# Kernel tuning notes

Hardware: AMD Instinct MI355X
Metric: run time of the kernel (lower is better)

The kernel has to match this reference:

```python
import jax, jax.numpy as jnp
from jax import lax
import numpy as np

DIM = 768      # model dim
NL = 12        # num mamba layers
DS = 16        # d_state
DI = 1536      # d_inner = 2*dim
DC = 4         # d_conv
P = 16         # patch size
IMG = 256
NP = (IMG // P) ** 2  # 256 patches
GS = 5         # KAN grid_size
SO = 3         # KAN spline_order
NK = NL // 3   # 4 KAN layers
BATCH = 32


def setup_inputs() -> dict:
    key = jax.random.key(0)
    ks = jax.random.split(key, 16)
    def n(k, shape, s=0.02):
        return jax.random.normal(k, shape, jnp.float32) * s
    return {
        "x": jax.random.normal(ks[0], (BATCH, 3, IMG, IMG), jnp.float32),
        "patch_w": n(ks[1], (DIM, 3, P, P)),
        "patch_b": jnp.zeros((DIM,), jnp.float32),
        "pos_embed": n(ks[2], (1, NP, DIM)),
        "in_proj_w": n(ks[3], (NL, 2 * DI, DIM)),
        "conv_w": n(ks[4], (NL, DI, 1, DC), 0.1),
        "conv_b": jnp.zeros((NL, DI), jnp.float32),
        "x_proj_w": n(ks[5], (NL, 2 * DS, DI)),
        "dt_proj_w": n(ks[6], (NL, DS, DI)),
        "dt_proj_b": jnp.zeros((NL, DS), jnp.float32),
        "A_log": jnp.tile(jnp.log(jnp.arange(1, DS + 1, dtype=jnp.float32)), (NL, 1)),
        "D_param": jnp.ones((NL, DI), jnp.float32),
        "out_proj_w": n(ks[7], (NL, DIM, DI)),
        "kan_base_w": n(ks[8], (NK, DIM, DIM)),
        "kan_coeff": n(ks[9], (NK, DIM, DIM, GS + SO), 0.1),
        "kan_bias": n(ks[10], (NK, DIM), 0.01),
        "norm_w": jnp.ones((DIM,), jnp.float32),
        "norm_b": jnp.zeros((DIM,), jnp.float32),
    }


def _mamba_block(x, in_w, cw, cb, xpw, dtw, dtb, alog, Dp, ow):
    Bsz, L, _ = x.shape
    xr = jnp.einsum('bld,ed->ble', x, in_w)              # [B,L,2*DI]
    x1, res = xr[..., :DI], xr[..., DI:]
    # causal depthwise conv (pad d_conv-1 on left, truncate to L)
    xc = lax.conv_general_dilated(
        x1.transpose(0, 2, 1), cw, (1,), [(DC - 1, 0)],
        feature_group_count=DI,
        dimension_numbers=('NCH', 'OIH', 'NCH')) + cb[None, :, None]
    x1 = jax.nn.silu(xc.transpose(0, 2, 1))              # [B,L,DI]
    x_dbl = jnp.einsum('bld,ed->ble', x1, xpw)           # [B,L,2*DS]
    Bp = x_dbl[..., DS:]                                 # dt half of x_proj is discarded (as in torch)
    dt = jax.nn.softplus(jnp.einsum('bld,nd->bln', x1, dtw) + dtb)  # [B,L,DS]
    A = -jnp.exp(alog)                                   # [DS]
    Ad = jnp.exp(A * dt)                                 # [B,L,DS]
    u = x1[..., :DI // DS].mean(-1)                      # [B,L]
    Bd = dt * Bp * u[..., None]                          # [B,L,DS]
    def step(s, ab):
        a, b = ab
        s = s * a + b
        return s, s
    _, ys = lax.scan(step, jnp.zeros((Bsz, DS), x.dtype),
                     (Ad.transpose(1, 0, 2), Bd.transpose(1, 0, 2)))
    y = ys.transpose(1, 0, 2)                            # [B,L,DS]
    y = jnp.repeat(y, DI // DS, axis=-1)                 # n -> (n d)
    y = y + x1 * Dp
    y = y * jax.nn.silu(res)
    return jnp.einsum('bld,ed->ble', y, ow)              # [B,L,DIM]


def _kan(xf, bw, coeff, bias):
    base = xf @ bw.T + bias
    grid = jnp.linspace(-1.0, 1.0, GS + 1)
    denom = grid[1:] - grid[:-1] + 1e-8
    xs = (xf[..., None] - grid[:-1]) / denom             # [M,DIM,GS]
    basis = jnp.where((xs >= 0) & (xs < 1), xs, 0.0)
    return base + jnp.einsum('bik,oik->bo', basis, coeff[:, :, :GS])


def reference(x, patch_w, patch_b, pos_embed, in_proj_w, conv_w, conv_b,
              x_proj_w, dt_proj_w, dt_proj_b, A_log, D_param, out_proj_w,
              kan_base_w, kan_coeff, kan_bias, norm_w, norm_b):
    Bsz = x.shape[0]
    h = lax.conv_general_dilated(
        x, patch_w, (P, P), 'VALID',
        dimension_numbers=('NCHW', 'OIHW', 'NCHW')) + patch_b[None, :, None, None]
    h = h.transpose(0, 2, 3, 1).reshape(Bsz, NP, DIM) + pos_embed
    for i in range(NL):
        h = _mamba_block(h, in_proj_w[i], conv_w[i], conv_b[i], x_proj_w[i],
                         dt_proj_w[i], dt_proj_b[i], A_log[i], D_param[i], out_proj_w[i])
        if i % 3 == 2 and i // 3 < NK:
            j = i // 3
            hf = h.reshape(-1, DIM)
            h = _kan(hf, kan_base_w[j], kan_coeff[j], kan_bias[j]).reshape(Bsz, NP, DIM) + h
    mu = h.mean(-1, keepdims=True)
    var = ((h - mu) ** 2).mean(-1, keepdims=True)
    return (h - mu) / jnp.sqrt(var + 1e-5) * norm_w + norm_b
```

## Files before the change

### kernel.cpp

```cpp
#include <hip/hip_runtime.h>

#define BATCH 32
#define NPATCH 256
#define MROWS (BATCH * NPATCH)
#define DIM 768
#define DI 1536
#define DS 16

typedef __bf16 bf16_t;
typedef __attribute__((ext_vector_type(8))) __bf16 bf16x8;
typedef __attribute__((ext_vector_type(4))) float floatx4;

__device__ __forceinline__ float bf2f(unsigned short u) {
    union { unsigned int i; float f; } v; v.i = ((unsigned int)u) << 16; return v.f;
}
__device__ __forceinline__ unsigned short f2bf(float f) {
    union { float f; unsigned int i; } u; u.f = f;
    unsigned int r = u.i + 0x7FFFu + ((u.i >> 16) & 1u);
    return (unsigned short)(r >> 16);
}
__device__ __forceinline__ float ldin(const void* p, int i, int bf) {
    if (bf) return bf2f(((const unsigned short*)p)[i]);
    return ((const float*)p)[i];
}
__device__ __forceinline__ float4 ldin4(const void* p, int i, int bf) {
    if (bf) {
        ushort4 u = *(const ushort4*)((const unsigned short*)p + i);
        return make_float4(bf2f(u.x), bf2f(u.y), bf2f(u.z), bf2f(u.w));
    }
    return *(const float4*)((const float*)p + i);
}
__device__ __forceinline__ float siluf(float x) { return x / (1.0f + expf(-x)); }

__global__ void detect_k(const void* alog, int* flag) {
    if (threadIdx.x == 0 && blockIdx.x == 0) {
        float v = ((const float*)alog)[1];
        flag[0] = (fabsf(v - 0.69314718f) < 0.01f) ? 0 : 1;
    }
}

__global__ __launch_bounds__(256) void cvt4_k(const int* __restrict__ flag,
                                              const void* __restrict__ in,
                                              unsigned short* __restrict__ out, int n4) {
    int i = blockIdx.x * 256 + threadIdx.x;
    if (i >= n4) return;
    float4 v = ldin4(in, i * 4, flag[0]);
    ushort4 o;
    o.x = f2bf(v.x); o.y = f2bf(v.y); o.z = f2bf(v.z); o.w = f2bf(v.w);
    *(ushort4*)(out + i * 4) = o;
}

__global__ __launch_bounds__(256) void kcoef_k(const int* __restrict__ flag,
                                               const void* __restrict__ co,
                                               bf16_t* __restrict__ out) {
    int idx = blockIdx.x * 256 + threadIdx.x;
    int bf = flag[0];
    int j = idx / (768 * 3840);
    int r = idx - j * (768 * 3840);
    int n = r / 3840;
    int kk = r - n * 3840;
    int i = kk / 5, k5 = kk - i * 5;
    out[idx] = (bf16_t)ldin(co, ((j * 768 + n) * 768 + i) * 8 + k5, bf);
}

__global__ __launch_bounds__(256) void wproj_k(const int* __restrict__ flag,
                                               const void* __restrict__ dtw,
                                               const void* __restrict__ xpw,
                                               bf16_t* __restrict__ w2) {
    int idx = blockIdx.x * 256 + threadIdx.x;
    int bf = flag[0];
    int i = idx / (128 * 1536);
    int r = idx - i * (128 * 1536);
    int n = r / 1536, k = r - n * 1536;
    float v;
    if (n < 16)       v = ldin(dtw, (i * 16 + n) * 1536 + k, bf);
    else if (n < 32)  v = ldin(xpw, (i * 32 + n) * 1536 + k, bf);
    else if (n == 32) v = (k < 96) ? (1.0f / 96.0f) : 0.0f;
    else              v = 0.0f;
    w2[idx] = (bf16_t)v;
}

__global__ __launch_bounds__(256) void cvtconv_k(const int* __restrict__ flag,
                                                 const void* __restrict__ cw,
                                                 bf16_t* __restrict__ cwr) {
    int idx = blockIdx.x * 256 + threadIdx.x;
    int bf = flag[0];
    int i = idx / (4 * 1536);
    int r = idx - i * (4 * 1536);
    int k = r / 1536, c = r - k * 1536;
    cwr[idx] = (bf16_t)ldin(cw, i * 1536 * 4 + c * 4 + k, bf);
}

__global__ __launch_bounds__(256) void basis_k(const bf16_t* __restrict__ h,
                                               bf16_t* __restrict__ bas) {
    int idx = blockIdx.x * 256 + threadIdx.x;
    int m = idx / 96, i8 = (idx - m * 96) * 8;
    bf16x8 hv = *(const bf16x8*)(h + (size_t)m * 768 + i8);
    union { bf16_t a[40]; bf16x8 v[5]; } ob;
#pragma unroll
    for (int ii = 0; ii < 8; ii++) {
        float xv = (float)hv[ii];
#pragma unroll
        for (int k5 = 0; k5 < 5; k5++) {
            float tt = (xv + 1.0f - 0.4f * (float)k5) * 2.5f;
            ob.a[ii * 5 + k5] = (bf16_t)((tt >= 0.0f && tt < 1.0f) ? tt : 0.0f);
        }
    }
    bf16_t* op = bas + (size_t)m * 3840 + (size_t)i8 * 5;
#pragma unroll
    for (int j = 0; j < 5; j++) *(bf16x8*)(op + j * 8) = ob.v[j];
}

__global__ __launch_bounds__(256) void im2col_k(const int* __restrict__ flag,
                                                const void* __restrict__ x,
                                                bf16_t* __restrict__ xp) {
    int idx = blockIdx.x * 256 + threadIdx.x;
    int bf = flag[0];
    int m = idx / 768, kc = idx - m * 768;
    int b = m >> 8, p = m & 255;
    int py = p >> 4, px = p & 15;
    int c = kc >> 8, rr = kc & 255;
    int ky = rr >> 4, kx = rr & 15;
    int src = ((b * 3 + c) * 256 + py * 16 + ky) * 256 + px * 16 + kx;
    xp[idx] = (bf16_t)ldin(x, src, bf);
}

template<int DBUF>
__global__ __launch_bounds__(256) void mgemm_t(
    const bf16_t* __restrict__ A, int lda,
    const bf16_t* __restrict__ W, int ldw,
    bf16_t* __restrict__ C, int ldc,
    int K, int mode, int gx,
    const int* __restrict__ flag,
    const void* __restrict__ bias, int boff,
    const void* __restrict__ aux, int aoff,
    const bf16_t* __restrict__ H, int ldh,
    float* __restrict__ dtu) {
    __shared__ bf16_t sm[DBUF ? 2 : 1][2 * 128 * 64];
    const int t = threadIdx.x;
    const int lane = t & 63, wave = t >> 6;
    const int wm = wave >> 1, wn = wave & 1;

    int m0, n0, kbeg, kend;
    if (mode == 5) {
        int mt = blockIdx.x >> 2, ks = blockIdx.x & 3;
        m0 = mt << 7; n0 = 0;
        int KS = K >> 2;
        kbeg = ks * KS; kend = kbeg + KS;
    } else {
        const int bid = blockIdx.x;
        const int xcd = bid & 7, l = bid >> 3;
        const int w = gx < 8 ? gx : 8;
        const int cb8 = w * 8;
        const int ch = l / cb8, rem = l - ch * cb8;
        const int mi = rem / w, ni = rem - mi * w;
        m0 = (xcd * 8 + mi) << 7;
        n0 = (ch * w + ni) << 7;
        kbeg = 0; kend = K;
    }

    const int srow = t >> 3;
    const int colperm = (((t & 7) ^ (srow & 7)) << 3);
    const bf16_t* gA[4]; const bf16_t* gB[4];
#pragma unroll
    for (int r = 0; r < 4; r++) {
        gA[r] = A + (size_t)(m0 + r * 32 + srow) * lda + colperm;
        gB[r] = W + (size_t)(n0 + r * 32 + srow) * ldw + colperm;
    }

    floatx4 acc[4][4];
#pragma unroll
    for (int i = 0; i < 4; i++)
#pragma unroll
        for (int j = 0; j < 4; j++) acc[i][j] = (floatx4){0.f, 0.f, 0.f, 0.f};

    const int kq = lane >> 4;
    const int mr = lane & 15;

    auto stage = [&](int buf, int kt) {
        char* sa = (char*)&sm[buf][0];
#pragma unroll
        for (int r = 0; r < 4; r++) {
            const int off = r * 4096 + wave * 1024;
            __builtin_amdgcn_global_load_lds(
                (const __attribute__((address_space(1))) unsigned int*)(gA[r] + kt),
                (__attribute__((address_space(3))) unsigned int*)(sa + off), 16, 0, 0);
            __builtin_amdgcn_global_load_lds(
                (const __attribute__((address_space(1))) unsigned int*)(gB[r] + kt),
                (__attribute__((address_space(3))) unsigned int*)(sa + 16384 + off), 16, 0, 0);
        }
    };

    auto compute = [&](int buf) {
        const bf16_t* sAc = &sm[buf][0];
        const bf16_t* sBc = sAc + 128 * 64;
#pragma unroll
        for (int half = 0; half < 2; half++) {
            const int cb = half * 4 + kq;
            if (mode == 5) {
                if (wn == 0) {
                    bf16x8 af[4], bw3[3];
#pragma unroll
                    for (int i = 0; i < 4; i++) {
                        int rw = wm * 64 + i * 16 + mr;
                        af[i] = *(const bf16x8*)(sAc + rw * 64 + ((cb ^ (rw & 7)) << 3));
                    }
#pragma unroll
                    for (int j = 0; j < 3; j++) {
                        int rw = j * 16 + mr;
                        bw3[j] = *(const bf16x8*)(sBc + rw * 64 + ((cb ^ (rw & 7)) << 3));
                    }
#pragma unroll
                    for (int i = 0; i < 4; i++)
#pragma unroll
                        for (int j = 0; j < 3; j++)
                            acc[i][j] = __builtin_amdgcn_mfma_f32_16x16x32_bf16(af[i], bw3[j], acc[i][j], 0, 0, 0);
                }
            } else {
                bf16x8 af[4], bw[4];
#pragma unroll
                for (int i = 0; i < 4; i++) {
                    int rw = wm * 64 + i * 16 + mr;
                    af[i] = *(const bf16x8*)(sAc + rw * 64 + ((cb ^ (rw & 7)) << 3));
                }
#pragma unroll
                for (int j = 0; j < 4; j++) {
                    int rw = wn * 64 + j * 16 + mr;
                    bw[j] = *(const bf16x8*)(sBc + rw * 64 + ((cb ^ (rw & 7)) << 3));
                }
#pragma unroll
                for (int i = 0; i < 4; i++)
#pragma unroll
                    for (int j = 0; j < 4; j++)
                        acc[i][j] = __builtin_amdgcn_mfma_f32_16x16x32_bf16(af[i], bw[j], acc[i][j], 0, 0, 0);
            }
        }
    };

    if (DBUF) {
        stage(0, kbeg);
        __syncthreads();
        int cur = 0;
        for (int kt = kbeg; kt < kend; kt += 64) {
            if (kt + 64 < kend) stage(cur ^ 1, kt + 64);
            compute(cur);
            __syncthreads();
            cur ^= 1;
        }
    } else {
        for (int kt = kbeg; kt < kend; kt += 64) {
            stage(0, kt);
            __syncthreads();
            compute(0);
            __syncthreads();
        }
    }

    const int col = lane & 15;
    const int rq = (lane >> 4) * 4;

    if (mode == 5) {
        if (wn == 0) {
            int ks = blockIdx.x & 3;
            float* dst = dtu + (size_t)ks * (MROWS * 64);
#pragma unroll
            for (int i = 0; i < 4; i++) {
#pragma unroll
                for (int reg = 0; reg < 4; reg++) {
                    int gm = m0 + wm * 64 + i * 16 + rq + reg;
#pragma unroll
                    for (int j = 0; j < 3; j++) {
                        int gn = j * 16 + col;
                        if (gn <= 32)
                            dst[(size_t)gm * 64 + gn] = acc[i][j][reg];
                    }
                }
            }
        }
        return;
    }

    const int bff = (mode == 1 || mode == 2) ? flag[0] : 0;
#pragma unroll
    for (int i = 0; i < 4; i++) {
#pragma unroll
        for (int reg = 0; reg < 4; reg++) {
            int gm = m0 + wm * 64 + i * 16 + rq + reg;
#pragma unroll
            for (int j = 0; j < 4; j++) {
                int gn = n0 + wn * 64 + j * 16 + col;
                float v = acc[i][j][reg];
                if (mode == 1) v += ldin(bias, boff + gn, bff) + ldin(aux, aoff + (gm & 255) * 768 + gn, bff);
                else if (mode == 2) v += ldin(bias, boff + gn, bff);
                else if (mode == 3) v += (float)C[(size_t)gm * ldc + gn] + (float)H[(size_t)gm * ldh + gn];
                C[(size_t)gm * ldc + gn] = (bf16_t)v;
            }
        }
    }
}

__global__ __launch_bounds__(256) void conv_k(const int* __restrict__ flag,
                                              const bf16_t* __restrict__ xr,
                                              const bf16_t* __restrict__ cwr,
                                              const void* __restrict__ cb, int cbo,
                                              bf16_t* __restrict__ xc) {
    int idx = blockIdx.x * 256 + threadIdx.x;
    int bf = flag[0];
    int m = idx / 192, c8 = (idx - m * 192) * 8;
    int l = m & 255;
    float acc[8];
    float4 b0 = ldin4(cb, cbo + c8, bf), b1 = ldin4(cb, cbo + c8 + 4, bf);
    acc[0] = b0.x; acc[1] = b0.y; acc[2] = b0.z; acc[3] = b0.w;
    acc[4] = b1.x; acc[5] = b1.y; acc[6] = b1.z; acc[7] = b1.w;
#pragma unroll
    for (int k = 0; k < 4; k++) {
        if (l + k - 3 >= 0) {
            bf16x8 xv = *(const bf16x8*)(xr + (size_t)(m + k - 3) * 3072 + c8);
            bf16x8 wv = *(const bf16x8*)(cwr + k * 1536 + c8);
#pragma unroll
            for (int j = 0; j < 8; j++) acc[j] += (float)xv[j] * (float)wv[j];
        }
    }
    bf16x8 o;
#pragma unroll
    for (int j = 0; j < 8; j++) o[j] = (bf16_t)siluf(acc[j]);
    *(bf16x8*)(xc + (size_t)m * 1536 + c8) = o;
}

__global__ __launch_bounds__(256) void scan_k(const int* __restrict__ flag,
                                              const float* __restrict__ dtu,
                                              const void* __restrict__ dtb, int dtbo,
                                              const void* __restrict__ alog, int alo,
                                              float* __restrict__ ys) {
    int wid = (blockIdx.x * 256 + threadIdx.x) >> 6;
    int lane = threadIdx.x & 63;
    int b = wid >> 4, s = wid & 15;
    int bf = flag[0];
    float dtbv = ldin(dtb, dtbo + s, bf);
    float Av = -expf(ldin(alog, alo + s, bf));
    const float* pb = dtu + (size_t)b * (256 * 64);
    float* yo = ys + (size_t)b * (256 * 16);
    float Aj[4], Bj[4];
    float A = 1.0f, Bv = 0.0f;
#pragma unroll
    for (int j = 0; j < 4; j++) {
        int l = lane * 4 + j;
        float rdt = dtbv, rBp = 0.0f, ru = 0.0f;
#pragma unroll
        for (int ks = 0; ks < 4; ks++) {
            const float* q = pb + (size_t)ks * (MROWS * 64) + (size_t)l * 64;
            rdt += q[s];
            rBp += q[16 + s];
            ru  += q[32];
        }
        float dt = (rdt > 20.0f) ? rdt : log1pf(expf(rdt));
        float a = expf(Av * dt);
        float bb = dt * rBp * ru;
        Bv = Bv * a + bb;
        A = A * a;
        Aj[j] = A; Bj[j] = Bv;
    }
#pragma unroll
    for (int off = 1; off < 64; off <<= 1) {
        float pa = __shfl_up(A, off);
        float pb2 = __shfl_up(Bv, off);
        if (lane >= off) { Bv = pb2 * A + Bv; A = pa * A; }
    }
    float ex = __shfl_up(Bv, 1);
    if (lane == 0) ex = 0.0f;
#pragma unroll
    for (int j = 0; j < 4; j++) {
        int l = lane * 4 + j;
        yo[l * 16 + s] = Aj[j] * ex + Bj[j];
    }
}

__global__ __launch_bounds__(256) void gate_k(const int* __restrict__ flag,
                                              const float* __restrict__ ys,
                                              bf16_t* __restrict__ xc,
                                              const bf16_t* __restrict__ xr,
                                              const void* __restrict__ Dp, int dpo) {
    int idx = blockIdx.x * 256 + threadIdx.x;
    int bf = flag[0];
    int m = idx / 192, d8 = (idx - m * 192) * 8;
    float yv = ys[m * 16 + d8 / 96];
    bf16x8 rv = *(const bf16x8*)(xr + (size_t)m * 3072 + 1536 + d8);
    bf16x8 xv = *(const bf16x8*)(xc + (size_t)m * 1536 + d8);
    float4 dp0 = ldin4(Dp, dpo + d8, bf), dp1 = ldin4(Dp, dpo + d8 + 4, bf);
    float dpv[8] = {dp0.x, dp0.y, dp0.z, dp0.w, dp1.x, dp1.y, dp1.z, dp1.w};
    bf16x8 o;
#pragma unroll
    for (int j = 0; j < 8; j++) {
        float v = yv + (float)xv[j] * dpv[j];
        o[j] = (bf16_t)(v * siluf((float)rv[j]));
    }
    *(bf16x8*)(xc + (size_t)m * 1536 + d8) = o;
}

__global__ __launch_bounds__(256) void lnorm_k(const int* __restrict__ flag,
                                               const bf16_t* __restrict__ h,
                                               const void* __restrict__ nw,
                                               const void* __restrict__ nb,
                                               void* __restrict__ out) {
    __shared__ float ls[4];
    int bf = flag[0];
    int m = blockIdx.x, t = threadIdx.x;
    const bf16_t* row = h + (size_t)m * 768;
    float v0 = (float)row[t], v1 = (float)row[t + 256], v2 = (float)row[t + 512];
    float s = v0 + v1 + v2;
#pragma unroll
    for (int o = 32; o; o >>= 1) s += __shfl_xor(s, o);
    if ((t & 63) == 0) ls[t >> 6] = s;
    __syncthreads();
    float mu = (ls[0] + ls[1] + ls[2] + ls[3]) * (1.0f / 768.0f);
    __syncthreads();
    float d0 = v0 - mu, d1 = v1 - mu, d2 = v2 - mu;
    float q = d0 * d0 + d1 * d1 + d2 * d2;
#pragma unroll
    for (int o = 32; o; o >>= 1) q += __shfl_xor(q, o);
    if ((t & 63) == 0) ls[t >> 6] = q;
    __syncthreads();
    float var = (ls[0] + ls[1] + ls[2] + ls[3]) * (1.0f / 768.0f);
    float inv = rsqrtf(var + 1e-5f);
    float vv[3] = {d0, d1, d2};
#pragma unroll
    for (int j = 0; j < 3; j++) {
        int colx = t + 256 * j;
        float o = vv[j] * inv * ldin(nw, colx, bf) + ldin(nb, colx, bf);
        size_t oi = (size_t)m * 768 + colx;
        if (bf) ((unsigned short*)out)[oi] = f2bf(o);
        else    ((float*)out)[oi] = o;
    }
}

extern "C" void kernel_launch(void* const* d_in, const int* in_sizes, int n_in,
                              void* d_out, int out_size, void* d_ws, size_t ws_size,
                              hipStream_t stream) {
    const void* x        = d_in[0];
    const void* patch_w  = d_in[1];
    const void* patch_b  = d_in[2];
    const void* pos      = d_in[3];
    const void* in_w     = d_in[4];
    const void* conv_w   = d_in[5];
    const void* conv_b   = d_in[6];
    const void* xpw      = d_in[7];
    const void* dtw      = d_in[8];
    const void* dtb      = d_in[9];
    const void* alog     = d_in[10];
    const void* Dp       = d_in[11];
    const void* out_w    = d_in[12];
    const void* kbw      = d_in[13];
    const void* kcoef    = d_in[14];
    const void* kbias    = d_in[15];
    const void* nw       = d_in[16];
    const void* nb       = d_in[17];

    char* base = (char*)d_ws;
    size_t off = 0;
    int* flag = (int*)base;                          off += 256;
    float* dtu  = (float*)(base + off);              off += (size_t)4 * MROWS * 64 * 4;
    float* ysb  = (float*)(base + off);              off += (size_t)MROWS * 16 * 4;
    bf16_t* hA  = (bf16_t*)(base + off);             off += (size_t)MROWS * DIM * 2;
    bf16_t* hB  = (bf16_t*)(base + off);             off += (size_t)MROWS * DIM * 2;
    bf16_t* xr  = (bf16_t*)(base + off);             off += (size_t)MROWS * 2 * DI * 2;
    bf16_t* xc  = (bf16_t*)(base + off);             off += (size_t)MROWS * DI * 2;
    bf16_t* wpatch = (bf16_t*)(base + off);          off += (size_t)DIM * DIM * 2;
    bf16_t* win  = (bf16_t*)(base + off);            off += (size_t)12 * 2 * DI * DIM * 2;
    bf16_t* wout = (bf16_t*)(base + off);            off += (size_t)12 * DIM * DI * 2;
    bf16_t* wkbw = (bf16_t*)(base + off);            off += (size_t)4 * DIM * DIM * 2;
    bf16_t* wkco = (bf16_t*)(base + off);            off += (size_t)4 * DIM * 3840 * 2;
    bf16_t* w2   = (bf16_t*)(base + off);            off += (size_t)12 * 128 * DI * 2;
    bf16_t* cwr  = (bf16_t*)(base + off);            off += (size_t)12 * 4 * DI * 2;
    bf16_t* basis = xr;
    bf16_t* im2c  = xr;

    detect_k<<<1, 64, 0, stream>>>(alog, flag);

    cvt4_k<<<(DIM * DIM / 4 + 255) / 256, 256, 0, stream>>>(flag, patch_w, (unsigned short*)wpatch, DIM * DIM / 4);
    cvt4_k<<<(12 * 2 * DI * DIM / 4 + 255) / 256, 256, 0, stream>>>(flag, in_w, (unsigned short*)win, 12 * 2 * DI * DIM / 4);
    cvt4_k<<<(12 * DIM * DI / 4 + 255) / 256, 256, 0, stream>>>(flag, out_w, (unsigned short*)wout, 12 * DIM * DI / 4);
    cvt4_k<<<(4 * DIM * DIM / 4 + 255) / 256, 256, 0, stream>>>(flag, kbw, (unsigned short*)wkbw, 4 * DIM * DIM / 4);
    kcoef_k<<<4 * DIM * 3840 / 256, 256, 0, stream>>>(flag, kcoef, wkco);
    wproj_k<<<12 * 128 * DI / 256, 256, 0, stream>>>(flag, dtw, xpw, w2);
    cvtconv_k<<<12 * 4 * DI / 256, 256, 0, stream>>>(flag, conv_w, cwr);

    im2col_k<<<(MROWS * DIM) / 256, 256, 0, stream>>>(flag, x, im2c);
    mgemm_t<1><<<6 * 64, 256, 0, stream>>>(
        im2c, DIM, wpatch, DIM, hA, DIM, DIM, 1, 6,
        flag, patch_b, 0, pos, 0, nullptr, 0, nullptr);

    bf16_t* hcur = hA;
    bf16_t* hoth = hB;
    for (int i = 0; i < 12; i++) {
        mgemm_t<0><<<24 * 64, 256, 0, stream>>>(
            hcur, DIM, win + (size_t)i * 2 * DI * DIM, DIM, xr, 2 * DI, DIM, 0, 24,
            flag, nullptr, 0, nullptr, 0, nullptr, 0, nullptr);
        conv_k<<<(MROWS * 192) / 256, 256, 0, stream>>>(
            flag, xr, cwr + (size_t)i * 4 * DI, conv_b, i * DI, xc);
        mgemm_t<1><<<256, 256, 0, stream>>>(
            xc, DI, w2 + (size_t)i * 128 * DI, DI, nullptr, 128, DI, 5, 1,
            flag, nullptr, 0, nullptr, 0, nullptr, 0, dtu);
        scan_k<<<128, 256, 0, stream>>>(flag, dtu, dtb, i * DS, alog, i * DS, ysb);
        gate_k<<<(MROWS * 192) / 256, 256, 0, stream>>>(
            flag, ysb, xc, xr, Dp, i * DI);
        mgemm_t<1><<<6 * 64, 256, 0, stream>>>(
            xc, DI, wout + (size_t)i * DIM * DI, DI, hcur, DIM, DI, 0, 6,
            flag, nullptr, 0, nullptr, 0, nullptr, 0, nullptr);
        if (i % 3 == 2) {
            int j = i / 3;
            mgemm_t<1><<<6 * 64, 256, 0, stream>>>(
                hcur, DIM, wkbw + (size_t)j * DIM * DIM, DIM, hoth, DIM, DIM, 2, 6,
                flag, kbias, j * DIM, nullptr, 0, nullptr, 0, nullptr);
            basis_k<<<(MROWS * 96) / 256, 256, 0, stream>>>(hcur, basis);
            mgemm_t<1><<<6 * 64, 256, 0, stream>>>(
                basis, 3840, wkco + (size_t)j * DIM * 3840, 3840, hoth, DIM, 3840, 3, 6,
                flag, nullptr, 0, nullptr, 0, hcur, DIM, nullptr);
            bf16_t* tmp = hcur; hcur = hoth; hoth = tmp;
        }
    }

    lnorm_k<<<MROWS, 256, 0, stream>>>(flag, hcur, nw, nb, d_out);
}
```

Baseline: 2.898 ms.

## Double-buffer all GEMMs and use partial vmcnt waits with raw barriers

```diff
diff --git a/kernel.cpp b/kernel.cpp
--- a/kernel.cpp
+++ b/kernel.cpp
@@ -125,8 +125,7 @@
     xp[idx] = (bf16_t)ldin(x, src, bf);
 }
 
-template<int DBUF>
-__global__ __launch_bounds__(256) void mgemm_t(
+__global__ __launch_bounds__(256) void mgemm_k(
     const bf16_t* __restrict__ A, int lda,
     const bf16_t* __restrict__ W, int ldw,
     bf16_t* __restrict__ C, int ldc,
@@ -136,7 +135,7 @@
     const void* __restrict__ aux, int aoff,
     const bf16_t* __restrict__ H, int ldh,
     float* __restrict__ dtu) {
-    __shared__ bf16_t sm[DBUF ? 2 : 1][2 * 128 * 64];
+    __shared__ bf16_t sm[2][2 * 128 * 64];
     const int t = threadIdx.x;
     const int lane = t & 63, wave = t >> 6;
     const int wm = wave >> 1, wn = wave & 1;
@@ -237,23 +236,19 @@
         }
     };
 
-    if (DBUF) {
-        stage(0, kbeg);
-        __syncthreads();
-        int cur = 0;
-        for (int kt = kbeg; kt < kend; kt += 64) {
-            if (kt + 64 < kend) stage(cur ^ 1, kt + 64);
-            compute(cur);
-            __syncthreads();
-            cur ^= 1;
-        }
-    } else {
-        for (int kt = kbeg; kt < kend; kt += 64) {
-            stage(0, kt);
-            __syncthreads();
-            compute(0);
-            __syncthreads();
-        }
+    stage(0, kbeg);
+    int cur = 0;
+    for (int kt = kbeg; kt < kend; kt += 64) {
+        if (kt + 64 < kend) {
+            stage(cur ^ 1, kt + 64);
+            asm volatile("s_waitcnt vmcnt(8)" ::: "memory");
+        } else {
+            asm volatile("s_waitcnt vmcnt(0)" ::: "memory");
+        }
+        asm volatile("s_barrier" ::: "memory");
+        compute(cur);
+        asm volatile("s_barrier" ::: "memory");
+        cur ^= 1;
     }
 
     const int col = lane & 15;
@@ -485,34 +480,34 @@
     cvtconv_k<<<12 * 4 * DI / 256, 256, 0, stream>>>(flag, conv_w, cwr);
 
     im2col_k<<<(MROWS * DIM) / 256, 256, 0, stream>>>(flag, x, im2c);
-    mgemm_t<1><<<6 * 64, 256, 0, stream>>>(
+    mgemm_k<<<6 * 64, 256, 0, stream>>>(
         im2c, DIM, wpatch, DIM, hA, DIM, DIM, 1, 6,
         flag, patch_b, 0, pos, 0, nullptr, 0, nullptr);
 
     bf16_t* hcur = hA;
     bf16_t* hoth = hB;
     for (int i = 0; i < 12; i++) {
-        mgemm_t<0><<<24 * 64, 256, 0, stream>>>(
+        mgemm_k<<<24 * 64, 256, 0, stream>>>(
             hcur, DIM, win + (size_t)i * 2 * DI * DIM, DIM, xr, 2 * DI, DIM, 0, 24,
             flag, nullptr, 0, nullptr, 0, nullptr, 0, nullptr);
         conv_k<<<(MROWS * 192) / 256, 256, 0, stream>>>(
             flag, xr, cwr + (size_t)i * 4 * DI, conv_b, i * DI, xc);
-        mgemm_t<1><<<256, 256, 0, stream>>>(
+        mgemm_k<<<256, 256, 0, stream>>>(
             xc, DI, w2 + (size_t)i * 128 * DI, DI, nullptr, 128, DI, 5, 1,
             flag, nullptr, 0, nullptr, 0, nullptr, 0, dtu);
         scan_k<<<128, 256, 0, stream>>>(flag, dtu, dtb, i * DS, alog, i * DS, ysb);
         gate_k<<<(MROWS * 192) / 256, 256, 0, stream>>>(
             flag, ysb, xc, xr, Dp, i * DI);
-        mgemm_t<1><<<6 * 64, 256, 0, stream>>>(
+        mgemm_k<<<6 * 64, 256, 0, stream>>>(
             xc, DI, wout + (size_t)i * DIM * DI, DI, hcur, DIM, DI, 0, 6,
             flag, nullptr, 0, nullptr, 0, nullptr, 0, nullptr);
         if (i % 3 == 2) {
             int j = i / 3;
-            mgemm_t<1><<<6 * 64, 256, 0, stream>>>(
+            mgemm_k<<<6 * 64, 256, 0, stream>>>(
                 hcur, DIM, wkbw + (size_t)j * DIM * DIM, DIM, hoth, DIM, DIM, 2, 6,
                 flag, kbias, j * DIM, nullptr, 0, nullptr, 0, nullptr);
             basis_k<<<(MROWS * 96) / 256, 256, 0, stream>>>(hcur, basis);
-            mgemm_t<1><<<6 * 64, 256, 0, stream>>>(
+            mgemm_k<<<6 * 64, 256, 0, stream>>>(
                 basis, 3840, wkco + (size_t)j * DIM * 3840, 3840, hoth, DIM, 3840, 3, 6,
                 flag, nullptr, 0, nullptr, 0, hcur, DIM, nullptr);
             bf16_t* tmp = hcur; hcur = hoth; hoth = tmp;
```

New measurement: 2.591 ms. 1.12x faster.
